# Kernel optimization log

Hardware: AMD Instinct MI355X
Metric: run time of the kernel (lower is better)

Reference implementation:

```python
import jax, jax.numpy as jnp
import numpy as np

B, S = 8, 512
HIDDEN = 513
SPATIAL = HIDDEN - 1           # 512
F = SPATIAL // 2 + 1           # 257 rfft bins
F2, F4 = 2 * F, 4 * F          # 514, 1028
IN_DIM = F2 + F2 + 2 * SPATIAL # 2052
MAX_STEPS = 20
TOL = 1e-3


def _ln(x, g, b):
    m = x.mean(-1, keepdims=True)
    v = ((x - m) ** 2).mean(-1, keepdims=True)
    return (x - m) * jax.lax.rsqrt(v + 1e-5) * g + b


def _freq_net(x, w1, b1, g, beta, w2, b2):
    # Linear -> LayerNorm -> GELU(exact) -> Linear -> Tanh
    h = jax.nn.gelu(_ln(x @ w1 + b1, g, beta), approximate=False)
    return jnp.tanh(h @ w2 + b2)


def _mlp(x, w1, b1, w2, b2):
    # Linear -> GELU(exact) -> Linear
    return jax.nn.gelu(x @ w1 + b1, approximate=False) @ w2 + b2


def setup_inputs() -> dict:
    key = jax.random.key(0)
    ks = jax.random.split(key, 16)
    def n(k, shape, s=0.05):
        return jax.random.normal(k, shape, jnp.float32) * s
    return dict(
        carrier_in=n(ks[0], (B, S, SPATIAL), 1.0),
        trajectory_in=n(ks[1], (B, S, SPATIAL), 1.0),
        source_pos=n(ks[2], (B, HIDDEN), 1.0),
        target_pos=n(ks[3], (B, HIDDEN), 1.0),
        cw1=n(ks[4], (IN_DIM, F4)), cb1=jnp.zeros(F4), cg=jnp.ones(F4), cbeta=jnp.zeros(F4),
        cw2=n(ks[5], (F4, F2)), cb2=jnp.zeros(F2),
        tw1=n(ks[6], (IN_DIM, F4)), tb1=jnp.zeros(F4), tg=jnp.ones(F4), tbeta=jnp.zeros(F4),
        tw2=n(ks[7], (F4, F2)), tb2=jnp.zeros(F2),
        freq_damping=jnp.linspace(0.95, 0.5, F).astype(jnp.float32),
        dw1=n(ks[8], (F2, F)), db1=jnp.zeros(F), dw2=n(ks[9], (F, 1)), db2=jnp.ones(1),
        sw1=n(ks[10], (F2, F // 2)), sb1=jnp.zeros(F // 2), sw2=n(ks[11], (F // 2, 1)), sb2=jnp.ones(1),
        carrier_scale=jnp.float32(0.1), trajectory_scale=jnp.float32(0.1),
    )


def reference(carrier_in, trajectory_in, source_pos, target_pos,
              cw1, cb1, cg, cbeta, cw2, cb2,
              tw1, tb1, tg, tbeta, tw2, tb2,
              freq_damping, dw1, db1, dw2, db2,
              sw1, sb1, sw2, sb2,
              carrier_scale, trajectory_scale):
    b, s, _ = carrier_in.shape
    src = jnp.broadcast_to(source_pos[:, None, :SPATIAL], (b, s, SPATIAL))
    tgt = jnp.broadcast_to(target_pos[:, None, :SPATIAL], (b, s, SPATIAL))

    def to_flat(x):  # rfft -> view_as_real -> flatten: [b,s,2F] (re,im interleaved)
        f = jnp.fft.rfft(x, axis=-1)
        return jnp.stack([f.real, f.imag], axis=-1).reshape(b, s, F2).astype(jnp.float32)

    c0 = to_flat(carrier_in)
    t0 = to_flat(trajectory_in)
    # torch: repeat(1,1,2).flatten -> tiled [d_0..d_{F-1}, d_0..d_{F-1}]
    damping = jnp.concatenate([freq_damping, freq_damping])

    def clamp10(x):
        nrm = jnp.linalg.norm(x)
        return jnp.where(nrm > 10.0, x * (10.0 / nrm), x)

    def step(carry, _):
        c, t, done = carry
        combined = jnp.concatenate([c, t, src, tgt], axis=-1)  # [b,s,IN_DIM]
        fc = _freq_net(combined, cw1, cb1, cg, cbeta, cw2, cb2)
        ft = _freq_net(combined, tw1, tb1, tg, tbeta, tw2, tb2)
        safe_c = jnp.nan_to_num(c, nan=0.0, posinf=1e6, neginf=-1e6)
        safe_t = jnp.nan_to_num(t, nan=0.0, posinf=1e6, neginf=-1e6)
        alpha_c = jax.nn.sigmoid(_mlp(safe_c, dw1, db1, dw2, db2))
        alpha_t = jax.nn.sigmoid(_mlp(safe_t, dw1, db1, dw2, db2))
        gamma = jax.nn.sigmoid(_mlp(safe_c, sw1, sb1, sw2, sb2)) + 0.5
        alpha_c = jnp.where(jnp.isnan(alpha_c), 0.0, alpha_c)
        alpha_t = jnp.where(jnp.isnan(alpha_t), 0.0, alpha_t)
        new_c = damping * c + gamma * alpha_c * carrier_scale * fc
        new_t = damping * t + gamma * alpha_t * trajectory_scale * ft
        dc = jnp.linalg.norm(new_c - c, axis=-1).mean()
        dt = jnp.linalg.norm(new_t - t, axis=-1).mean()
        conv = (dc < TOL) & (dt < TOL)
        # on convergence the torch loop breaks BEFORE the norm clamp
        out_c = jnp.where(conv, new_c, clamp10(new_c))
        out_t = jnp.where(conv, new_t, clamp10(new_t))
        out_c = jnp.where(done, c, out_c)
        out_t = jnp.where(done, t, out_t)
        return (out_c, out_t, done | conv), None

    (cf, tf, _), _ = jax.lax.scan(step, (c0, t0, jnp.array(False)), None, length=MAX_STEPS)

    def to_spatial(x):
        xr = x.reshape(b, s, F, 2)
        return jnp.fft.irfft(xr[..., 0] + 1j * xr[..., 1], n=SPATIAL, axis=-1).astype(jnp.float32)

    return to_spatial(cf), to_spatial(tf)


if __name__ == '__main__':
    out = reference(**setup_inputs())
    print(out[0].shape, out[1].shape)
```

## Files before the change

### kernel.cpp

```cpp
#include <hip/hip_runtime.h>
#include <hip/hip_bf16.h>
#include <math.h>

typedef __hip_bfloat16 bf16;
using s16x8 = __attribute__((ext_vector_type(8))) short;
using f32x4 = __attribute__((ext_vector_type(4))) float;
typedef __attribute__((address_space(1))) const unsigned int gu32;
typedef __attribute__((address_space(3))) unsigned int lu32;

#define RTOT 4096
#define XCT  1056
#define NT1  2176
#define HLD  2176
#define KH   1088
#define CLD  640
#define KDP  576
#define NDC  512
#define F2E  514
#define SP   512
#define YZS  16

__device__ __forceinline__ float gelu_ex(float x) {
    return 0.5f * x * (1.0f + erff(x * 0.70710678118654752f));
}
__device__ __forceinline__ float sigm(float x) { return 1.0f / (1.0f + expf(-x)); }
__device__ __forceinline__ float n2n(float x) {
    if (isnan(x)) return 0.0f;
    if (isinf(x)) return x > 0.0f ? 1e6f : -1e6f;
    return x;
}
__device__ __forceinline__ unsigned short bfb(float x) {
    __hip_bfloat16 h = __float2bfloat16(x);
    return *(unsigned short*)&h;
}
__device__ __forceinline__ unsigned packbf(float x, float y) {
    return (unsigned)bfb(x) | ((unsigned)bfb(y) << 16);
}
__device__ __forceinline__ void glds16(const bf16* g, short* l) {
    __builtin_amdgcn_global_load_lds((gu32*)g, (lu32*)l, 16, 0, 0);
}

template<int EPI>
__global__ __launch_bounds__(256)
void gemm_bt(const bf16* __restrict__ A, int lda,
             const bf16* __restrict__ Bt, int ldb,
             float* __restrict__ C, int ldc,
             const float* __restrict__ bias, int bias_ld, int ktiles,
             long zA, long zB, long zC, long zBias)
{
    A    += (long)blockIdx.z * zA;
    Bt   += (long)blockIdx.z * zB;
    C    += (long)blockIdx.z * zC;
    bias += (long)blockIdx.z * zBias;

    __shared__ __align__(16) short As[128 * 32];
    __shared__ __align__(16) short Bs[128 * 32];
    const int tid  = threadIdx.x;
    const int lane = tid & 63;
    const int wave = tid >> 6;
    const int l15  = lane & 15, kl = lane >> 4;
    const long mb = (long)blockIdx.x * 128;
    const long nb = (long)blockIdx.y * 128;
    const int wr = (wave >> 1) * 64;
    const int wc = (wave & 1) * 64;

    f32x4 acc[4][4] = {};

    const int grp_r = lane >> 2;
    const int gcol  = (lane & 3) * 8;
    const bf16* gA0 = A  + (mb + wave * 32 + grp_r) * (long)lda + gcol;
    const bf16* gA1 = gA0 + 16 * (long)lda;
    const bf16* gB0 = Bt + (nb + wave * 32 + grp_r) * (long)ldb + gcol;
    const bf16* gB1 = gB0 + 16 * (long)ldb;
    short* lA0 = &As[(wave * 32) * 32];
    short* lA1 = &As[(wave * 32 + 16) * 32];
    short* lB0 = &Bs[(wave * 32) * 32];
    short* lB1 = &Bs[(wave * 32 + 16) * 32];

    for (int kt = 0; kt < ktiles; ++kt) {
        const long ko = (long)kt * 32;
        __syncthreads();
        glds16(gA0 + ko, lA0);
        glds16(gA1 + ko, lA1);
        glds16(gB0 + ko, lB0);
        glds16(gB1 + ko, lB1);
        __syncthreads();
        s16x8 af[4], bfr[4];
#pragma unroll
        for (int m = 0; m < 4; ++m) {
            int ar = wr + m * 16 + l15;
            af[m] = *reinterpret_cast<const s16x8*>(&As[ar * 32 + kl * 8]);
        }
#pragma unroll
        for (int n = 0; n < 4; ++n) {
            int br = wc + n * 16 + l15;
            bfr[n] = *reinterpret_cast<const s16x8*>(&Bs[br * 32 + kl * 8]);
        }
#pragma unroll
        for (int m = 0; m < 4; ++m)
#pragma unroll
            for (int n = 0; n < 4; ++n)
                acc[m][n] = __builtin_amdgcn_mfma_f32_16x16x32_bf16(af[m], bfr[n], acc[m][n], 0, 0, 0);
    }

    const float* brow = bias + (bias_ld ? (long)(mb >> 9) * bias_ld : 0);
#pragma unroll
    for (int m = 0; m < 4; ++m) {
        const long grow0 = mb + wr + m * 16 + kl * 4;
#pragma unroll
        for (int n = 0; n < 4; ++n) {
            const long gcol2 = nb + wc + n * 16 + l15;
            const float bb = brow[gcol2];
            f32x4 v = acc[m][n];
#pragma unroll
            for (int r = 0; r < 4; ++r) {
                float x = v[r] + bb;
                if (EPI == 1) x = tanhf(x);
                else if (EPI == 2) x = gelu_ex(x);
                C[(grow0 + r) * (long)ldc + gcol2] = x;
            }
        }
    }
}

__global__ __launch_bounds__(256)
void sgemm_bt(const float* __restrict__ A, int lda,
              const float* __restrict__ Bt, int ldb,
              float* __restrict__ C, int ldc, int ktiles)
{
    __shared__ float As[16][68];
    __shared__ float Bs[16][68];
    const int tid = threadIdx.x;
    const int tx = tid & 15, ty = tid >> 4;
    const int lr = tid >> 2, lc = (tid & 3) * 4;
    const long mb = (long)blockIdx.x * 64, nb = (long)blockIdx.y * 64;
    float acc[4][4] = {};
    const float* Ap = A  + (mb + lr) * (long)lda + lc;
    const float* Bp = Bt + (nb + lr) * (long)ldb + lc;
    for (int kt = 0; kt < ktiles; ++kt) {
        float4 av = *(const float4*)(Ap + kt * 16);
        float4 bv = *(const float4*)(Bp + kt * 16);
        __syncthreads();
        As[lc + 0][lr] = av.x; As[lc + 1][lr] = av.y;
        As[lc + 2][lr] = av.z; As[lc + 3][lr] = av.w;
        Bs[lc + 0][lr] = bv.x; Bs[lc + 1][lr] = bv.y;
        Bs[lc + 2][lr] = bv.z; Bs[lc + 3][lr] = bv.w;
        __syncthreads();
#pragma unroll
        for (int kk = 0; kk < 16; ++kk) {
            float4 a = *(const float4*)&As[kk][ty * 4];
            float4 b = *(const float4*)&Bs[kk][tx * 4];
            acc[0][0] = fmaf(a.x, b.x, acc[0][0]); acc[0][1] = fmaf(a.x, b.y, acc[0][1]);
            acc[0][2] = fmaf(a.x, b.z, acc[0][2]); acc[0][3] = fmaf(a.x, b.w, acc[0][3]);
            acc[1][0] = fmaf(a.y, b.x, acc[1][0]); acc[1][1] = fmaf(a.y, b.y, acc[1][1]);
            acc[1][2] = fmaf(a.y, b.z, acc[1][2]); acc[1][3] = fmaf(a.y, b.w, acc[1][3]);
            acc[2][0] = fmaf(a.z, b.x, acc[2][0]); acc[2][1] = fmaf(a.z, b.y, acc[2][1]);
            acc[2][2] = fmaf(a.z, b.z, acc[2][2]); acc[2][3] = fmaf(a.z, b.w, acc[2][3]);
            acc[3][0] = fmaf(a.w, b.x, acc[3][0]); acc[3][1] = fmaf(a.w, b.y, acc[3][1]);
            acc[3][2] = fmaf(a.w, b.z, acc[3][2]); acc[3][3] = fmaf(a.w, b.w, acc[3][3]);
        }
    }
#pragma unroll
    for (int i = 0; i < 4; ++i) {
        float4 st = { acc[i][0], acc[i][1], acc[i][2], acc[i][3] };
        *(float4*)&C[(mb + ty * 4 + i) * (long)ldc + nb + tx * 4] = st;
    }
}

__global__ void build_tables(float* __restrict__ RT, float* __restrict__ IT)
{
    long idx = (long)blockIdx.x * 256 + threadIdx.x;
    const double W = 6.283185307179586476925286766559005768 / 512.0;
    if (idx < 640L * 512) {
        int r = (int)(idx >> 9), n = (int)(idx & 511);
        float v = 0.f;
        if (r < F2E) {
            int bin = r >> 1;
            int m = (bin * n) & 511;
            double ang = W * m;
            v = (r & 1) ? (float)(-sin(ang)) : (float)cos(ang);
        }
        RT[idx] = v;
    } else {
        long j2 = idx - 640L * 512;
        if (j2 < 512L * 640) {
            int n = (int)(j2 / 640), j = (int)(j2 % 640);
            float v = 0.f;
            if (j < F2E) {
                int bin = j >> 1;
                int m = (bin * n) & 511;
                double ang = W * m;
                bool edge = (bin == 0 || bin == 256);
                double ck = edge ? 1.0 : 2.0;
                if (j & 1) v = edge ? 0.f : (float)(-ck * sin(ang) / 512.0);
                else       v = (float)(ck * cos(ang) / 512.0);
            }
            IT[j2] = v;
        }
    }
}

__global__ void build_damp(float* damp, const float* __restrict__ fd)
{
    int i = blockIdx.x * 256 + threadIdx.x;
    if (i < F2E) damp[i] = fd[i < 257 ? i : i - 257];
}

__global__ void ybase_part(const float* __restrict__ srcp, const float* __restrict__ tgtp,
                           const float* __restrict__ cw1, const float* __restrict__ tw1,
                           float* __restrict__ Yp)
{
    const int n = blockIdx.x * 256 + threadIdx.x;
    const int b = blockIdx.y, z = blockIdx.z;
    if (n >= NT1) return;
    float acc = 0.f;
    if (n < 2056) {
        const bool isT = (n >= 1028);
        const int nn = isT ? n - 1028 : n;
        const float* w = isT ? tw1 : cw1;
        const float* s = srcp + b * 513;
        const float* t = tgtp + b * 513;
        const int k0 = z * (512 / YZS);
        for (int k = k0; k < k0 + 512 / YZS; ++k) {
            acc = fmaf(s[k], w[(size_t)(1028 + k) * 1028 + nn], acc);
            acc = fmaf(t[k], w[(size_t)(1540 + k) * 1028 + nn], acc);
        }
    }
    Yp[((size_t)z * 8 + b) * NT1 + n] = acc;
}

__global__ void ybase_reduce(const float* __restrict__ Yp,
                             const float* __restrict__ cb1, const float* __restrict__ tb1,
                             float* __restrict__ Yb)
{
    const int n = blockIdx.x * 256 + threadIdx.x;
    const int b = blockIdx.y;
    if (n >= NT1) return;
    float acc = 0.f;
    if (n < 2056) acc = (n < 1028) ? cb1[n] : tb1[n - 1028];
    for (int z = 0; z < YZS; ++z) acc += Yp[((size_t)z * 8 + b) * NT1 + n];
    Yb[b * NT1 + n] = acc;
}

__global__ void wprep(bf16* __restrict__ dst, int ldk,
                      const float* s0, int K0, int N0, int r00,
                      const float* s1, int K1, int N1, int r01)
{
    int r = blockIdx.x;
    int k = blockIdx.y * 256 + threadIdx.x;
    if (k >= ldk) return;
    float v = 0.f;
    if (s0 && r >= r00 && r < r00 + N0 && k < K0) v = s0[(long)k * N0 + (r - r00)];
    if (s1 && r >= r01 && r < r01 + N1 && k < K1) v = s1[(long)k * N1 + (r - r01)];
    dst[(long)r * ldk + k] = __float2bfloat16(v);
}

__global__ void bias_fill(float* __restrict__ dst, int n,
                          const float* s0, int l0, int o0,
                          const float* s1, int l1, int o1)
{
    int i = blockIdx.x * 256 + threadIdx.x;
    if (i >= n) return;
    float v = 0.f;
    if (s0 && i >= o0 && i < o0 + l0) v = s0[i - o0];
    if (s1 && i >= o1 && i < o1 + l1) v = s1[i - o1];
    dst[i] = v;
}

__global__ void initconv(const float* __restrict__ cb, const float* __restrict__ tb,
                         bf16* __restrict__ X, bf16* __restrict__ Cb, bf16* __restrict__ Tb)
{
    int row = blockIdx.x;
    for (int j = threadIdx.x; j < F2E; j += 256) {
        float cv = cb[(long)row * CLD + j], tv = tb[(long)row * CLD + j];
        X[(long)row * XCT + j]        = __float2bfloat16(cv);
        X[(long)row * XCT + 514 + j]  = __float2bfloat16(tv);
        Cb[(long)row * KDP + j] = __float2bfloat16(n2n(cv));
        Tb[(long)row * KDP + j] = __float2bfloat16(n2n(tv));
    }
}

__global__ void xpad_zero(bf16* __restrict__ X)
{
    int row = blockIdx.x;
    int j = 1028 + threadIdx.x;
    if (j < XCT) X[(long)row * XCT + j] = __float2bfloat16(0.f);
}

__global__ __launch_bounds__(256)
void ln_gelu(const float* __restrict__ Y, bf16* __restrict__ H,
             const float* __restrict__ cg, const float* __restrict__ cbeta,
             const float* __restrict__ tg, const float* __restrict__ tbeta)
{
    const int lane = threadIdx.x & 63, wave = threadIdx.x >> 6;
    const int p = blockIdx.x * 4 + wave;
    const int row = p >> 1, net = p & 1;
    const float4* y4 = (const float4*)(Y + (long)row * NT1 + net * 1028);
    float4 v[4], vt = {0.f, 0.f, 0.f, 0.f};
    float s = 0.f;
#pragma unroll
    for (int k = 0; k < 4; ++k) {
        v[k] = y4[lane + k * 64];
        s += v[k].x + v[k].y + v[k].z + v[k].w;
    }
    if (lane == 0) { vt = y4[256]; s += vt.x + vt.y + vt.z + vt.w; }
#pragma unroll
    for (int o = 1; o < 64; o <<= 1) s += __shfl_xor(s, o, 64);
    const float mean = s * (1.0f / 1028.0f);
    float vs = 0.f;
#pragma unroll
    for (int k = 0; k < 4; ++k) {
        float a = v[k].x - mean, b = v[k].y - mean, c = v[k].z - mean, d = v[k].w - mean;
        vs += a * a + b * b + c * c + d * d;
    }
    if (lane == 0) {
        float a = vt.x - mean, b = vt.y - mean, c = vt.z - mean, d = vt.w - mean;
        vs += a * a + b * b + c * c + d * d;
    }
#pragma unroll
    for (int o = 1; o < 64; o <<= 1) vs += __shfl_xor(vs, o, 64);
    const float rs = rsqrtf(vs * (1.0f / 1028.0f) + 1e-5f);
    const float4* g4 = (const float4*)(net ? tg : cg);
    const float4* b4 = (const float4*)(net ? tbeta : cbeta);
    bf16* h = H + (long)row * HLD + (long)net * KH;
#pragma unroll
    for (int k = 0; k < 4; ++k) {
        int j = lane + k * 64;
        float4 gv = g4[j], bv = b4[j];
        ushort4 o;
        o.x = bfb(gelu_ex((v[k].x - mean) * rs * gv.x + bv.x));
        o.y = bfb(gelu_ex((v[k].y - mean) * rs * gv.y + bv.y));
        o.z = bfb(gelu_ex((v[k].z - mean) * rs * gv.z + bv.z));
        o.w = bfb(gelu_ex((v[k].w - mean) * rs * gv.w + bv.w));
        *(ushort4*)(&h[j * 4]) = o;
    }
    if (lane == 0) {
        float4 gv = g4[256], bv = b4[256];
        ushort4 o;
        o.x = bfb(gelu_ex((vt.x - mean) * rs * gv.x + bv.x));
        o.y = bfb(gelu_ex((vt.y - mean) * rs * gv.y + bv.y));
        o.z = bfb(gelu_ex((vt.z - mean) * rs * gv.z + bv.z));
        o.w = bfb(gelu_ex((vt.w - mean) * rs * gv.w + bv.w));
        *(ushort4*)(&h[1024]) = o;
    }
}

__global__ __launch_bounds__(256)
void fused_update(const float* __restrict__ Hd,
                  const float* __restrict__ dw2, const float* __restrict__ db2,
                  const float* __restrict__ sw2, const float* __restrict__ sb2,
                  const float* __restrict__ c, const float* __restrict__ t,
                  const float* __restrict__ fc, const float* __restrict__ ft,
                  float* __restrict__ nc, float* __restrict__ nt,
                  const float* __restrict__ damp,
                  const float* __restrict__ csc, const float* __restrict__ tsc,
                  float* __restrict__ part)
{
    __shared__ float red[16];
    const int tid = threadIdx.x, lane = tid & 63, wave = tid >> 6;
    const int row = blockIdx.x * 4 + wave;

    const float* hc = Hd + (long)row * NDC;
    const float* ht = Hd + (long)(4096 + row) * NDC;
    float s1 = 0.f, s2 = 0.f, s3 = 0.f;
#pragma unroll
    for (int k = 0; k < 4; ++k) {
        int j = lane + k * 64;
        s1 += hc[j] * dw2[j];
        s3 += ht[j] * dw2[j];
    }
    if (lane == 0) { s1 += hc[256] * dw2[256]; s3 += ht[256] * dw2[256]; }
#pragma unroll
    for (int k = 0; k < 2; ++k) {
        int j = lane + k * 64;
        s2 += hc[257 + j] * sw2[j];
    }
#pragma unroll
    for (int o = 1; o < 64; o <<= 1) {
        s1 += __shfl_xor(s1, o, 64);
        s2 += __shfl_xor(s2, o, 64);
        s3 += __shfl_xor(s3, o, 64);
    }
    float a  = sigm(s1 + db2[0]);
    float at = sigm(s3 + db2[0]);
    float g  = sigm(s2 + sb2[0]) + 0.5f;
    if (isnan(a))  a  = 0.f;
    if (isnan(at)) at = 0.f;
    const float gac = g * a  * csc[0];
    const float gat = g * at * tsc[0];

    const float2* c2  = (const float2*)(c  + (long)row * CLD);
    const float2* t2  = (const float2*)(t  + (long)row * CLD);
    const float2* fc2 = (const float2*)(fc + (long)row * CLD);
    const float2* ft2 = (const float2*)(ft + (long)row * CLD);
    float2* nc2 = (float2*)(nc + (long)row * CLD);
    float2* nt2 = (float2*)(nt + (long)row * CLD);
    const float2* d2 = (const float2*)damp;
    float sdc = 0.f, snc = 0.f, sdt = 0.f, snt = 0.f;
#pragma unroll
    for (int k = 0; k < 4; ++k) {
        int j = lane + k * 64;
        float2 dv = d2[j];
        float2 cv = c2[j], fv = fc2[j];
        float2 ncv = { dv.x * cv.x + gac * fv.x, dv.y * cv.y + gac * fv.y };
        nc2[j] = ncv;
        float dx = ncv.x - cv.x, dy = ncv.y - cv.y;
        sdc += dx * dx + dy * dy;
        snc += ncv.x * ncv.x + ncv.y * ncv.y;
        float2 tv = t2[j], gv = ft2[j];
        float2 ntv = { dv.x * tv.x + gat * gv.x, dv.y * tv.y + gat * gv.y };
        nt2[j] = ntv;
        dx = ntv.x - tv.x; dy = ntv.y - tv.y;
        sdt += dx * dx + dy * dy;
        snt += ntv.x * ntv.x + ntv.y * ntv.y;
    }
    if (lane == 0) {
        float2 dv = d2[256];
        float2 cv = c2[256], fv = fc2[256];
        float2 ncv = { dv.x * cv.x + gac * fv.x, dv.y * cv.y + gac * fv.y };
        nc2[256] = ncv;
        float dx = ncv.x - cv.x, dy = ncv.y - cv.y;
        sdc += dx * dx + dy * dy;
        snc += ncv.x * ncv.x + ncv.y * ncv.y;
        float2 tv = t2[256], gv = ft2[256];
        float2 ntv = { dv.x * tv.x + gat * gv.x, dv.y * tv.y + gat * gv.y };
        nt2[256] = ntv;
        dx = ntv.x - tv.x; dy = ntv.y - tv.y;
        sdt += dx * dx + dy * dy;
        snt += ntv.x * ntv.x + ntv.y * ntv.y;
    }
#pragma unroll
    for (int o = 1; o < 64; o <<= 1) {
        sdc += __shfl_xor(sdc, o, 64);
        snc += __shfl_xor(snc, o, 64);
        sdt += __shfl_xor(sdt, o, 64);
        snt += __shfl_xor(snt, o, 64);
    }
    if (lane == 0) {
        red[wave * 4 + 0] = sqrtf(sdc);
        red[wave * 4 + 1] = sqrtf(sdt);
        red[wave * 4 + 2] = snc;
        red[wave * 4 + 3] = snt;
    }
    __syncthreads();
    if (tid < 4)
        part[tid * 1024 + blockIdx.x] =
            red[0 * 4 + tid] + red[1 * 4 + tid] + red[2 * 4 + tid] + red[3 * 4 + tid];
}

__global__ __launch_bounds__(256)
void update3(float* __restrict__ c, float* __restrict__ t,
             const float* __restrict__ nc, const float* __restrict__ nt,
             bf16* __restrict__ X, bf16* __restrict__ Cb, bf16* __restrict__ Tb,
             const float* __restrict__ part, float* __restrict__ scal, int step)
{
    __shared__ float red[4];
    const int tid = threadIdx.x, lane = tid & 63, wave = tid >> 6;
    {
        const float* pq = part + wave * 1024;
        float s = 0.f;
#pragma unroll
        for (int k = 0; k < 16; ++k) s += pq[lane + k * 64];
#pragma unroll
        for (int o = 1; o < 64; o <<= 1) s += __shfl_xor(s, o, 64);
        if (lane == 0) red[wave] = s;
    }
    __syncthreads();
    const float done = scal[step];
    const float dc = red[0] * (1.0f / 4096.0f);
    const float dt = red[1] * (1.0f / 4096.0f);
    const bool conv = (dc < 1e-3f) && (dt < 1e-3f);
    if (blockIdx.x == 0 && tid == 0)
        scal[step + 1] = (done != 0.f || conv) ? 1.f : 0.f;
    if (done != 0.f) return;
    const float nrc = sqrtf(red[2]);
    const float nrt = sqrtf(red[3]);
    const float sc = conv ? 1.f : (nrc > 10.f ? 10.f / nrc : 1.f);
    const float st = conv ? 1.f : (nrt > 10.f ? 10.f / nrt : 1.f);

    const int row = blockIdx.x * 4 + wave;
    const float2* nc2 = (const float2*)(nc + (long)row * CLD);
    const float2* nt2 = (const float2*)(nt + (long)row * CLD);
    float2* c2 = (float2*)(c + (long)row * CLD);
    float2* t2 = (float2*)(t + (long)row * CLD);
    bf16* xr = X  + (long)row * XCT;
    bf16* cb = Cb + (long)row * KDP;
    bf16* tb = Tb + (long)row * KDP;
#pragma unroll
    for (int k = 0; k < 5; ++k) {
        int j = lane + k * 64;
        if (k == 4 && lane > 0) break;
        float2 cv = nc2[j]; cv.x *= sc; cv.y *= sc;
        float2 tv = nt2[j]; tv.x *= st; tv.y *= st;
        c2[j] = cv;
        t2[j] = tv;
        *(unsigned*)(xr + j * 2)       = packbf(cv.x, cv.y);
        *(unsigned*)(xr + 514 + j * 2) = packbf(tv.x, tv.y);
        *(unsigned*)(cb + j * 2) = packbf(n2n(cv.x), n2n(cv.y));
        *(unsigned*)(tb + j * 2) = packbf(n2n(tv.x), n2n(tv.y));
    }
}

extern "C" void kernel_launch(void* const* d_in, const int* in_sizes, int n_in,
                              void* d_out, int out_size, void* d_ws, size_t ws_size,
                              hipStream_t stream)
{
    (void)in_sizes; (void)n_in; (void)out_size; (void)ws_size;
    const float* carrier = (const float*)d_in[0];
    const float* traj    = (const float*)d_in[1];
    const float* srcp    = (const float*)d_in[2];
    const float* tgtp    = (const float*)d_in[3];
    const float* cw1 = (const float*)d_in[4];  const float* cb1 = (const float*)d_in[5];
    const float* cg  = (const float*)d_in[6];  const float* cbe = (const float*)d_in[7];
    const float* cw2 = (const float*)d_in[8];  const float* cb2 = (const float*)d_in[9];
    const float* tw1 = (const float*)d_in[10]; const float* tb1 = (const float*)d_in[11];
    const float* tg  = (const float*)d_in[12]; const float* tbe = (const float*)d_in[13];
    const float* tw2 = (const float*)d_in[14]; const float* tb2 = (const float*)d_in[15];
    const float* fd  = (const float*)d_in[16];
    const float* dw1 = (const float*)d_in[17]; const float* db1 = (const float*)d_in[18];
    const float* dw2 = (const float*)d_in[19]; const float* db2 = (const float*)d_in[20];
    const float* sw1 = (const float*)d_in[21]; const float* sb1 = (const float*)d_in[22];
    const float* sw2 = (const float*)d_in[23]; const float* sb2 = (const float*)d_in[24];
    const float* csc = (const float*)d_in[25]; const float* tsc = (const float*)d_in[26];

    char* p = (char*)d_ws;
    size_t off = 0;
    auto take = [&](size_t bytes) { size_t o = off; off += (bytes + 255) & ~(size_t)255; return o; };
    bf16*  Xct  = (bf16*) (p + take((size_t)RTOT * XCT * 2));
    bf16*  W1ct = (bf16*) (p + take((size_t)NT1 * XCT * 2));
    float* Y    = (float*)(p + take((size_t)RTOT * NT1 * 4));
    bf16*  H    = (bf16*) (p + take((size_t)RTOT * HLD * 2));
    bf16*  W2t  = (bf16*) (p + take((size_t)1280 * KH * 2));
    bf16*  Wdc  = (bf16*) (p + take((size_t)NDC * KDP * 2));
    float* Ybase= (float*)(p + take((size_t)8 * NT1 * 4));
    float* Ypart= (float*)(p + take((size_t)YZS * 8 * NT1 * 4));
    float* b2c  = (float*)(p + take(1280 * 4));
    float* bdc  = (float*)(p + take(NDC * 4));
    float* RT   = (float*)(p + take(640L * 512 * 4));
    float* IT   = (float*)(p + take(512L * 640 * 4));
    float* damp = (float*)(p + take(F2E * 4));
    float* cbuf = (float*)(p + take((size_t)RTOT * CLD * 4));
    float* tbuf = (float*)(p + take((size_t)RTOT * CLD * 4));
    float* ncb  = (float*)(p + take((size_t)RTOT * CLD * 4));
    float* ntb  = (float*)(p + take((size_t)RTOT * CLD * 4));
    float* fcb  = (float*)(p + take((size_t)2 * RTOT * CLD * 4));
    float* ftb  = fcb + (size_t)RTOT * CLD;
    bf16*  Cbb  = (bf16*) (p + take((size_t)2 * RTOT * KDP * 2));
    bf16*  Tbb  = Cbb + (size_t)RTOT * KDP;
    float* Hd   = (float*)(p + take((size_t)2 * RTOT * NDC * 4));
    float* part = (float*)(p + take(4096 * 4));
    float* scal = (float*)(p + take(1024));

    hipMemsetAsync(scal, 0, 1024, stream);

    build_tables<<<2560, 256, 0, stream>>>(RT, IT);
    build_damp<<<3, 256, 0, stream>>>(damp, fd);
    ybase_part<<<dim3(9, 8, YZS), 256, 0, stream>>>(srcp, tgtp, cw1, tw1, Ypart);
    ybase_reduce<<<dim3(9, 8), 256, 0, stream>>>(Ypart, cb1, tb1, Ybase);
    wprep<<<dim3(NT1, 5), 256, 0, stream>>>(W1ct, XCT, cw1, 1028, 1028, 0, tw1, 1028, 1028, 1028);
    wprep<<<dim3(1280, 5), 256, 0, stream>>>(W2t, KH, cw2, 1028, 514, 0, tw2, 1028, 514, 640);
    wprep<<<dim3(NDC, 3), 256, 0, stream>>>(Wdc, KDP, dw1, 514, 257, 0, sw1, 514, 128, 257);
    bias_fill<<<5, 256, 0, stream>>>(b2c, 1280, cb2, 514, 0, tb2, 514, 640);
    bias_fill<<<2, 256, 0, stream>>>(bdc, NDC, db1, 257, 0, sb1, 128, 257);
    xpad_zero<<<RTOT, 32, 0, stream>>>(Xct);

    sgemm_bt<<<dim3(64, 10), 256, 0, stream>>>(carrier, SP, RT, SP, cbuf, CLD, 32);
    sgemm_bt<<<dim3(64, 10), 256, 0, stream>>>(traj,    SP, RT, SP, tbuf, CLD, 32);
    initconv<<<RTOT, 256, 0, stream>>>(cbuf, tbuf, Xct, Cbb, Tbb);

    for (int s = 0; s < 20; ++s) {
        gemm_bt<0><<<dim3(32, 17), 256, 0, stream>>>(Xct, XCT, W1ct, XCT, Y, NT1,
                                                     Ybase, NT1, 33, 0, 0, 0, 0);
        ln_gelu<<<2048, 256, 0, stream>>>(Y, H, cg, cbe, tg, tbe);
        gemm_bt<1><<<dim3(32, 5, 2), 256, 0, stream>>>(H, HLD, W2t, KH, fcb, CLD,
                                                       b2c, 0, 34,
                                                       (long)KH, (long)640 * KH,
                                                       (long)RTOT * CLD, 640);
        gemm_bt<2><<<dim3(64, 4), 256, 0, stream>>>(Cbb, KDP, Wdc, KDP, Hd, NDC,
                                                    bdc, 0, 18, 0, 0, 0, 0);
        fused_update<<<1024, 256, 0, stream>>>(Hd, dw2, db2, sw2, sb2,
                                               cbuf, tbuf, fcb, ftb, ncb, ntb,
                                               damp, csc, tsc, part);
        update3<<<1024, 256, 0, stream>>>(cbuf, tbuf, ncb, ntb, Xct, Cbb, Tbb,
                                          part, scal, s);
    }

    float* out = (float*)d_out;
    sgemm_bt<<<dim3(64, 8), 256, 0, stream>>>(cbuf, CLD, IT, CLD, out, SP, 40);
    sgemm_bt<<<dim3(64, 8), 256, 0, stream>>>(tbuf, CLD, IT, CLD, out + (size_t)RTOT * SP, SP, 40);
}
```

Before: 3.133 ms.

## Double-buffer LDS tiles in bf16 GEMM and use narrower N tiles for small GEMMs

The bf16 GEMM kernel now keeps two LDS buffers and issues the global-to-LDS load for the next K tile before running the MFMAs on the current one, which removes one barrier per iteration and overlaps memory with compute. A BNT template parameter adds a 64-wide N tile, used by the second freq-net GEMM and the damping/step GEMM to double their block counts and fill more CUs. The cost is double the LDS footprint, which may reduce occupancy. There is also a possible race: the prefetch into the other buffer is asynchronous and nothing waits on it before the trailing barrier, unless the compiler inserts a vmcnt wait there.

```diff
diff --git a/kernel.cpp b/kernel.cpp
--- a/kernel.cpp
+++ b/kernel.cpp
@@ -40,7 +40,7 @@
     __builtin_amdgcn_global_load_lds((gu32*)g, (lu32*)l, 16, 0, 0);
 }
 
-template<int EPI>
+template<int EPI, int BNT>
 __global__ __launch_bounds__(256)
 void gemm_bt(const bf16* __restrict__ A, int lda,
              const bf16* __restrict__ Bt, int ldb,
@@ -53,54 +53,59 @@
     C    += (long)blockIdx.z * zC;
     bias += (long)blockIdx.z * zBias;
 
-    __shared__ __align__(16) short As[128 * 32];
-    __shared__ __align__(16) short Bs[128 * 32];
+    constexpr int NC = BNT / 32;
+    __shared__ __align__(16) short As[2][128 * 32];
+    __shared__ __align__(16) short Bs[2][BNT * 32];
     const int tid  = threadIdx.x;
     const int lane = tid & 63;
     const int wave = tid >> 6;
     const int l15  = lane & 15, kl = lane >> 4;
     const long mb = (long)blockIdx.x * 128;
-    const long nb = (long)blockIdx.y * 128;
+    const long nb = (long)blockIdx.y * BNT;
     const int wr = (wave >> 1) * 64;
-    const int wc = (wave & 1) * 64;
-
-    f32x4 acc[4][4] = {};
+    const int wc = (wave & 1) * (BNT / 2);
+
+    f32x4 acc[4][NC] = {};
 
     const int grp_r = lane >> 2;
     const int gcol  = (lane & 3) * 8;
     const bf16* gA0 = A  + (mb + wave * 32 + grp_r) * (long)lda + gcol;
     const bf16* gA1 = gA0 + 16 * (long)lda;
-    const bf16* gB0 = Bt + (nb + wave * 32 + grp_r) * (long)ldb + gcol;
+    const int brow0 = (BNT == 128) ? wave * 32 : wave * 16;
+    const bf16* gB0 = Bt + (nb + brow0 + grp_r) * (long)ldb + gcol;
     const bf16* gB1 = gB0 + 16 * (long)ldb;
-    short* lA0 = &As[(wave * 32) * 32];
-    short* lA1 = &As[(wave * 32 + 16) * 32];
-    short* lB0 = &Bs[(wave * 32) * 32];
-    short* lB1 = &Bs[(wave * 32 + 16) * 32];
-
+
+    auto stage = [&](int buf, int kt) {
+        const long ko = (long)kt * 32;
+        glds16(gA0 + ko, &As[buf][(wave * 32) * 32]);
+        glds16(gA1 + ko, &As[buf][(wave * 32 + 16) * 32]);
+        glds16(gB0 + ko, &Bs[buf][brow0 * 32]);
+        if (BNT == 128) glds16(gB1 + ko, &Bs[buf][(brow0 + 16) * 32]);
+    };
+
+    stage(0, 0);
+    __syncthreads();
+    int cur = 0;
     for (int kt = 0; kt < ktiles; ++kt) {
-        const long ko = (long)kt * 32;
-        __syncthreads();
-        glds16(gA0 + ko, lA0);
-        glds16(gA1 + ko, lA1);
-        glds16(gB0 + ko, lB0);
-        glds16(gB1 + ko, lB1);
-        __syncthreads();
-        s16x8 af[4], bfr[4];
+        if (kt + 1 < ktiles) stage(cur ^ 1, kt + 1);
+        s16x8 af[4], bfr[NC];
 #pragma unroll
         for (int m = 0; m < 4; ++m) {
             int ar = wr + m * 16 + l15;
-            af[m] = *reinterpret_cast<const s16x8*>(&As[ar * 32 + kl * 8]);
-        }
-#pragma unroll
-        for (int n = 0; n < 4; ++n) {
+            af[m] = *reinterpret_cast<const s16x8*>(&As[cur][ar * 32 + kl * 8]);
+        }
+#pragma unroll
+        for (int n = 0; n < NC; ++n) {
             int br = wc + n * 16 + l15;
-            bfr[n] = *reinterpret_cast<const s16x8*>(&Bs[br * 32 + kl * 8]);
+            bfr[n] = *reinterpret_cast<const s16x8*>(&Bs[cur][br * 32 + kl * 8]);
         }
 #pragma unroll
         for (int m = 0; m < 4; ++m)
 #pragma unroll
-            for (int n = 0; n < 4; ++n)
+            for (int n = 0; n < NC; ++n)
                 acc[m][n] = __builtin_amdgcn_mfma_f32_16x16x32_bf16(af[m], bfr[n], acc[m][n], 0, 0, 0);
+        __syncthreads();
+        cur ^= 1;
     }
 
     const float* brow = bias + (bias_ld ? (long)(mb >> 9) * bias_ld : 0);
@@ -108,7 +113,7 @@
     for (int m = 0; m < 4; ++m) {
         const long grow0 = mb + wr + m * 16 + kl * 4;
 #pragma unroll
-        for (int n = 0; n < 4; ++n) {
+        for (int n = 0; n < NC; ++n) {
             const long gcol2 = nb + wc + n * 16 + l15;
             const float bb = brow[gcol2];
             f32x4 v = acc[m][n];
@@ -569,15 +574,15 @@
     initconv<<<RTOT, 256, 0, stream>>>(cbuf, tbuf, Xct, Cbb, Tbb);
 
     for (int s = 0; s < 20; ++s) {
-        gemm_bt<0><<<dim3(32, 17), 256, 0, stream>>>(Xct, XCT, W1ct, XCT, Y, NT1,
-                                                     Ybase, NT1, 33, 0, 0, 0, 0);
+        gemm_bt<0, 128><<<dim3(32, 17), 256, 0, stream>>>(Xct, XCT, W1ct, XCT, Y, NT1,
+                                                          Ybase, NT1, 33, 0, 0, 0, 0);
         ln_gelu<<<2048, 256, 0, stream>>>(Y, H, cg, cbe, tg, tbe);
-        gemm_bt<1><<<dim3(32, 5, 2), 256, 0, stream>>>(H, HLD, W2t, KH, fcb, CLD,
-                                                       b2c, 0, 34,
-                                                       (long)KH, (long)640 * KH,
-                                                       (long)RTOT * CLD, 640);
-        gemm_bt<2><<<dim3(64, 4), 256, 0, stream>>>(Cbb, KDP, Wdc, KDP, Hd, NDC,
-                                                    bdc, 0, 18, 0, 0, 0, 0);
+        gemm_bt<1, 64><<<dim3(32, 10, 2), 256, 0, stream>>>(H, HLD, W2t, KH, fcb, CLD,
+                                                            b2c, 0, 34,
+                                                            (long)KH, (long)640 * KH,
+                                                            (long)RTOT * CLD, 640);
+        gemm_bt<2, 64><<<dim3(64, 8), 256, 0, stream>>>(Cbb, KDP, Wdc, KDP, Hd, NDC,
+                                                        bdc, 0, 18, 0, 0, 0, 0);
         fused_update<<<1024, 256, 0, stream>>>(Hd, dw2, db2, sw2, sb2,
                                                cbuf, tbuf, fcb, ftb, ncb, ntb,
                                                damp, csc, tsc, part);
```

After: 2.692 ms. 14.1% less time.
